# Performance work log

Measured on AMD Instinct MI355X. Metric: run time of the kernel, lower is better.

## Reference

```python
import jax, jax.numpy as jnp
import numpy as np

NG, N, NFG, NFR, NFP, B = 4, 64, 1024, 256, 256, 2048
SCALE = 1.0 / float(np.sqrt(NFR + NFP))
EPS = 1e-5  # torch LayerNorm default


def setup_inputs() -> dict:
    key = jax.random.key(0)
    k = jax.random.split(key, 4)
    x = jax.random.normal(k[0], (B, N, NFG), dtype=jnp.float32)
    # per-graph params stacked over NG for vectorized computation
    Wt = jax.random.normal(k[1], (NG, NFR, NFG), dtype=jnp.float32) * 0.02
    bt = jnp.zeros((NG, NFR), dtype=jnp.float32)
    Wp = jax.random.normal(k[2], (NG, NFR, NFG), dtype=jnp.float32) * 0.02
    bp = jnp.zeros((NG, NFR), dtype=jnp.float32)
    Wg = jax.random.normal(k[3], (NG, NFG, NFG), dtype=jnp.float32) * 0.02  # [out,in]
    gamma = jnp.ones((NG, NFG), dtype=jnp.float32)
    beta = jnp.zeros((NG, NFG), dtype=jnp.float32)
    return {"x": x, "Wt": Wt, "bt": bt, "Wp": Wp, "bp": bp,
            "Wg": Wg, "gamma": gamma, "beta": beta}


def reference(x, Wt, bt, Wp, bp, Wg, gamma, beta):
    # theta/phi projections, vectorized over NG graphs: [G,B,N,R]
    theta = jnp.einsum('bnf,grf->gbnr', x, Wt) + bt[:, None, None, :]
    phi = jnp.einsum('bnf,grf->gbnr', x, Wp) + bp[:, None, None, :]
    # original computes sim=theta@phi^T then .sum(2); identical math:
    # relation[b,n] = theta[b,n] . sum_m phi[b,m]  (avoids the NxN matrix)
    phi_sum = phi.sum(axis=2)                                  # [G,B,R]
    relation = jnp.einsum('gbnr,gbr->gbn', theta, phi_sum) * SCALE
    w = jax.nn.softmax(relation, axis=2)                       # softmax over boxes N
    # attention-weighted aggregation over boxes -> [G,B,NFG]
    agg = jnp.einsum('gbn,bnf->gbf', w, x)
    # GCN linear (no bias): [G,B,NFG]
    h = jnp.einsum('gbf,gof->gbo', agg, Wg)
    # LayerNorm over feature dim, per graph
    mu = h.mean(axis=-1, keepdims=True)
    var = ((h - mu) ** 2).mean(axis=-1, keepdims=True)
    h = (h - mu) * jax.lax.rsqrt(var + EPS) * gamma[:, None, :] + beta[:, None, :]
    h = jax.nn.relu(h)
    # mean over the NG graphs; restore keepdim axis -> [B,1,NFG]
    return h.mean(axis=0)[:, None, :]
```

## Files before the change

kernel.cpp:

```cpp
#include <hip/hip_runtime.h>
#include <hip/hip_bf16.h>

typedef __attribute__((ext_vector_type(4))) float f4;
typedef __attribute__((ext_vector_type(4))) float f32x4;
typedef __attribute__((ext_vector_type(8))) short short8;
typedef __attribute__((ext_vector_type(2))) unsigned int u32x2;
typedef __attribute__((ext_vector_type(4))) unsigned int u32x4;
typedef unsigned int u32;
typedef unsigned short u16;

#define SCALE_F 0.04419417382415922f

__device__ inline u16 f2bf(float f) {
  u32 u = __float_as_uint(f);
  u32 r = u + 0x7FFFu + ((u >> 16) & 1u);
  return (u16)(r >> 16);
}
__device__ inline float bflo(u32 u) { return __uint_as_float(u << 16); }
__device__ inline float bfhi(u32 u) { return __uint_as_float(u & 0xFFFF0000u); }

#define GLD16(gsrc, ldst)                                                     \
  __builtin_amdgcn_global_load_lds(                                           \
      (const __attribute__((address_space(1))) void*)(gsrc),                  \
      (__attribute__((address_space(3))) void*)(ldst), 16, 0, 0)

__global__ __launch_bounds__(256) void k0_cvt(const float* __restrict__ src,
                                              u16* __restrict__ dst) {
  int i = blockIdx.x * 256 + threadIdx.x;
  const f4* s = (const f4*)src;
  f4 a = s[(size_t)i * 2];
  f4 b = s[(size_t)i * 2 + 1];
  u32x4 p;
  p[0] = (u32)f2bf(a[0]) | ((u32)f2bf(a[1]) << 16);
  p[1] = (u32)f2bf(a[2]) | ((u32)f2bf(a[3]) << 16);
  p[2] = (u32)f2bf(b[0]) | ((u32)f2bf(b[1]) << 16);
  p[3] = (u32)f2bf(b[2]) | ((u32)f2bf(b[3]) << 16);
  *(u32x4*)(dst + (size_t)i * 8) = p;
}

__global__ __launch_bounds__(256) void k0_wt(const float* __restrict__ Wt,
                                             u16* __restrict__ Wtt) {
  const int g = blockIdx.z;
  const int f0 = blockIdx.x * 64, r0 = blockIdx.y * 64;
  __shared__ u16 tile[64][66];
  const int t = threadIdx.x;
  const float* src = Wt + ((size_t)g * 256 + r0) * 1024 + f0;
#pragma unroll
  for (int i = 0; i < 16; ++i) {
    int idx = t + i * 256;
    int rl = idx >> 6, fl = idx & 63;
    tile[fl][rl] = f2bf(src[rl * 1024 + fl]);
  }
  __syncthreads();
  u16* dst = Wtt + ((size_t)g * 1024 + f0) * 256 + r0;
#pragma unroll
  for (int i = 0; i < 4; ++i) {
    int idx = t + i * 256;
    int fl = idx >> 4, rq = idx & 15;
    u32x2 p;
    p[0] = (u32)tile[fl][rq * 4]     | ((u32)tile[fl][rq * 4 + 1] << 16);
    p[1] = (u32)tile[fl][rq * 4 + 2] | ((u32)tile[fl][rq * 4 + 3] << 16);
    *(u32x2*)(dst + fl * 256 + rq * 4) = p;
  }
}

__global__ __launch_bounds__(256) void k1_colsum(const float* __restrict__ x,
                                                 u16* __restrict__ xs16) {
  int b = blockIdx.x, t = threadIdx.x;
  const float* xb = x + (size_t)b * (64 * 1024);
  f4 acc = {0.f, 0.f, 0.f, 0.f};
#pragma unroll 8
  for (int n = 0; n < 64; ++n)
    acc += *(const f4*)(xb + n * 1024 + t * 4);
  u32x2 p;
  p[0] = (u32)f2bf(acc[0]) | ((u32)f2bf(acc[1]) << 16);
  p[1] = (u32)f2bf(acc[2]) | ((u32)f2bf(acc[3]) << 16);
  *(u32x2*)(xs16 + (size_t)b * 1024 + t * 4) = p;
}

__global__ __launch_bounds__(256) void k2_gemm(const u16* __restrict__ A,
                                               const u16* __restrict__ Bt,
                                               const float* __restrict__ bp,
                                               u16* __restrict__ C) {
  const int n0 = blockIdx.x * 128, m0 = blockIdx.y * 128;
  __shared__ u16 Al[128 * 32];
  __shared__ u16 Bl[128 * 32];
  const int t = threadIdx.x;
  const int w = t >> 6, l = t & 63;
  const int wr = w >> 1, wc = w & 1;
  const int lr = l & 15, lh = l >> 4;
  f32x4 acc[4][4] = {};
  for (int kt = 0; kt < 1024; kt += 32) {
#pragma unroll
    for (int j = 0; j < 2; ++j) {
      int idx = t + j * 256;
      int row = idx >> 2, sl = idx & 3;
      GLD16(A + (size_t)(m0 + row) * 1024 + kt + sl * 8, Al + idx * 8);
      GLD16(Bt + (size_t)(n0 + row) * 1024 + kt + sl * 8, Bl + idx * 8);
    }
    __syncthreads();
    short8 af[4], bfr[4];
#pragma unroll
    for (int m = 0; m < 4; ++m)
      af[m] = *(const short8*)(Al + (wr * 64 + m * 16 + lr) * 32 + lh * 8);
#pragma unroll
    for (int n = 0; n < 4; ++n)
      bfr[n] = *(const short8*)(Bl + (wc * 64 + n * 16 + lr) * 32 + lh * 8);
#pragma unroll
    for (int m = 0; m < 4; ++m)
#pragma unroll
      for (int n = 0; n < 4; ++n)
        acc[m][n] = __builtin_amdgcn_mfma_f32_16x16x32_bf16(af[m], bfr[n],
                                                            acc[m][n], 0, 0, 0);
    __syncthreads();
  }
#pragma unroll
  for (int m = 0; m < 4; ++m)
#pragma unroll
    for (int n = 0; n < 4; ++n) {
      int col = n0 + wc * 64 + n * 16 + lr;
      float bb = 64.0f * bp[col];
#pragma unroll
      for (int j = 0; j < 4; ++j)
        C[(size_t)(m0 + wr * 64 + m * 16 + lh * 4 + j) * 1024 + col] =
            f2bf(acc[m][n][j] + bb);
    }
}

__global__ __launch_bounds__(256) void k3_gemm(const u16* __restrict__ A,
                                               const u16* __restrict__ Btt,
                                               float* __restrict__ V) {
  const int g = blockIdx.z;
  const int n0 = blockIdx.x * 128, m0 = blockIdx.y * 128;
  const u16* Bg = Btt + (size_t)g * 1024 * 256;
  __shared__ u16 Al[128 * 32];
  __shared__ u16 Bl[128 * 32];
  const int t = threadIdx.x;
  const int w = t >> 6, l = t & 63;
  const int wr = w >> 1, wc = w & 1;
  const int lr = l & 15, lh = l >> 4;
  f32x4 acc[4][4] = {};
  for (int kt = 0; kt < 256; kt += 32) {
#pragma unroll
    for (int j = 0; j < 2; ++j) {
      int idx = t + j * 256;
      int row = idx >> 2, sl = idx & 3;
      GLD16(A + (size_t)(m0 + row) * 1024 + g * 256 + kt + sl * 8, Al + idx * 8);
      GLD16(Bg + (size_t)(n0 + row) * 256 + kt + sl * 8, Bl + idx * 8);
    }
    __syncthreads();
    short8 af[4], bfr[4];
#pragma unroll
    for (int m = 0; m < 4; ++m)
      af[m] = *(const short8*)(Al + (wr * 64 + m * 16 + lr) * 32 + lh * 8);
#pragma unroll
    for (int n = 0; n < 4; ++n)
      bfr[n] = *(const short8*)(Bl + (wc * 64 + n * 16 + lr) * 32 + lh * 8);
#pragma unroll
    for (int m = 0; m < 4; ++m)
#pragma unroll
      for (int n = 0; n < 4; ++n)
        acc[m][n] = __builtin_amdgcn_mfma_f32_16x16x32_bf16(af[m], bfr[n],
                                                            acc[m][n], 0, 0, 0);
    __syncthreads();
  }
  float* Vg = V + (size_t)g * 2048 * 1024;
#pragma unroll
  for (int m = 0; m < 4; ++m)
#pragma unroll
    for (int n = 0; n < 4; ++n)
#pragma unroll
      for (int j = 0; j < 4; ++j)
        Vg[(size_t)(m0 + wr * 64 + m * 16 + lh * 4 + j) * 1024 +
           (n0 + wc * 64 + n * 16 + lr)] = acc[m][n][j];
}

#define K4_LDS (131072 + 16384 + 8192 + 1024)
__global__ __launch_bounds__(1024) void k4_fused(const float* __restrict__ x,
                                                 const float* __restrict__ V,
                                                 u16* __restrict__ aggb) {
  extern __shared__ char sm[];
  char* xl = sm;
  float* vl = (float*)(sm + 131072);
  float* relp = (float*)(sm + 131072 + 16384);
  float* wsm = (float*)(sm + 131072 + 16384 + 8192);
  const int t = threadIdx.x;
  const int b = blockIdx.x;
  const float* xb = x + (size_t)b * 65536;

  f4 va = *(const f4*)(V + ((size_t)(t >> 8) * 2048 + b) * 1024 + (t & 255) * 4);
  f4 xr[8];
#pragma unroll
  for (int i = 0; i < 8; ++i) {
    int idx = i * 1024 + t;
    xr[i] = *(const f4*)(xb + (idx >> 8) * 1024 + (idx & 255) * 4);
  }
  *(f4*)(vl + t * 4) = va;
#pragma unroll
  for (int i = 0; i < 8; ++i) {
    int idx = i * 1024 + t;
    int row = idx >> 8, col4 = idx & 255;
    u32 p0 = (u32)f2bf(xr[i][0]) | ((u32)f2bf(xr[i][1]) << 16);
    u32 p1 = (u32)f2bf(xr[i][2]) | ((u32)f2bf(xr[i][3]) << 16);
    int slot = col4 >> 1, half = col4 & 1;
    char* dst = xl + row * 2048 + ((slot ^ (row & 7)) << 4) + half * 8;
    ((u32*)dst)[0] = p0;
    ((u32*)dst)[1] = p1;
  }
  f4 xr2[8];
#pragma unroll
  for (int i = 0; i < 8; ++i) {
    int idx = 8192 + i * 1024 + t;
    xr2[i] = *(const f4*)(xb + (idx >> 8) * 1024 + (idx & 255) * 4);
  }
  asm volatile("s_waitcnt lgkmcnt(0)" ::: "memory");
  __builtin_amdgcn_s_barrier();

  {
    const int h = t >> 7, g = (t >> 5) & 3, n = t & 31;
    const char* xrow = xl + n * 2048;
    const float* vg = vl + g * 1024 + h * 128;
    const int sw = n & 7;
    float racc = 0.f;
#pragma unroll
    for (int f8 = 0; f8 < 16; ++f8) {
      int slot = h * 16 + f8;
      u32x4 xp = *(const u32x4*)(xrow + ((slot ^ sw) << 4));
      f4 v0 = *(const f4*)(vg + f8 * 8);
      f4 v1 = *(const f4*)(vg + f8 * 8 + 4);
      racc = fmaf(bflo(xp[0]), v0[0], racc);
      racc = fmaf(bfhi(xp[0]), v0[1], racc);
      racc = fmaf(bflo(xp[1]), v0[2], racc);
      racc = fmaf(bfhi(xp[1]), v0[3], racc);
      racc = fmaf(bflo(xp[2]), v1[0], racc);
      racc = fmaf(bfhi(xp[2]), v1[1], racc);
      racc = fmaf(bflo(xp[3]), v1[2], racc);
      racc = fmaf(bfhi(xp[3]), v1[3], racc);
    }
    relp[t] = racc;
  }
#pragma unroll
  for (int i = 0; i < 8; ++i) {
    int idx = 8192 + i * 1024 + t;
    int row = idx >> 8, col4 = idx & 255;
    u32 p0 = (u32)f2bf(xr2[i][0]) | ((u32)f2bf(xr2[i][1]) << 16);
    u32 p1 = (u32)f2bf(xr2[i][2]) | ((u32)f2bf(xr2[i][3]) << 16);
    int slot = col4 >> 1, half = col4 & 1;
    char* dst = xl + row * 2048 + ((slot ^ (row & 7)) << 4) + half * 8;
    ((u32*)dst)[0] = p0;
    ((u32*)dst)[1] = p1;
  }
  asm volatile("s_waitcnt lgkmcnt(0)" ::: "memory");
  __builtin_amdgcn_s_barrier();

  {
    const int h = t >> 7, g = (t >> 5) & 3, n = 32 + (t & 31);
    const char* xrow = xl + n * 2048;
    const float* vg = vl + g * 1024 + h * 128;
    const int sw = n & 7;
    float racc = 0.f;
#pragma unroll
    for (int f8 = 0; f8 < 16; ++f8) {
      int slot = h * 16 + f8;
      u32x4 xp = *(const u32x4*)(xrow + ((slot ^ sw) << 4));
      f4 v0 = *(const f4*)(vg + f8 * 8);
      f4 v1 = *(const f4*)(vg + f8 * 8 + 4);
      racc = fmaf(bflo(xp[0]), v0[0], racc);
      racc = fmaf(bfhi(xp[0]), v0[1], racc);
      racc = fmaf(bflo(xp[1]), v0[2], racc);
      racc = fmaf(bfhi(xp[1]), v0[3], racc);
      racc = fmaf(bflo(xp[2]), v1[0], racc);
      racc = fmaf(bfhi(xp[2]), v1[1], racc);
      racc = fmaf(bflo(xp[3]), v1[2], racc);
      racc = fmaf(bfhi(xp[3]), v1[3], racc);
    }
    relp[1024 + t] = racc;
  }
  __syncthreads();

  if (t < 256) {
    const int g = t >> 6, n = t & 63;
    const float* base = (n < 32) ? (relp + g * 32 + (n & 31))
                                 : (relp + 1024 + g * 32 + (n & 31));
    float rel = 0.f;
#pragma unroll
    for (int h = 0; h < 8; ++h) rel += base[h * 128];
    rel *= SCALE_F;
    float mx = rel;
#pragma unroll
    for (int o = 32; o > 0; o >>= 1) mx = fmaxf(mx, __shfl_xor(mx, o, 64));
    float e = __expf(rel - mx);
    float s = e;
#pragma unroll
    for (int o = 32; o > 0; o >>= 1) s += __shfl_xor(s, o, 64);
    wsm[t] = e / s;
  }
  __syncthreads();

  {
    const int g = t >> 8, fb4 = t & 255;
    const float* wg = wsm + g * 64;
    const int slot = fb4 >> 1, half = fb4 & 1;
    float a0 = 0, a1 = 0, a2 = 0, a3 = 0;
#pragma unroll 8
    for (int n = 0; n < 64; ++n) {
      float w = wg[n];
      u32x2 xp = *(const u32x2*)(xl + n * 2048 + ((slot ^ (n & 7)) << 4) + half * 8);
      a0 = fmaf(bflo(xp[0]), w, a0);
      a1 = fmaf(bfhi(xp[0]), w, a1);
      a2 = fmaf(bflo(xp[1]), w, a2);
      a3 = fmaf(bfhi(xp[1]), w, a3);
    }
    u32x2 p;
    p[0] = (u32)f2bf(a0) | ((u32)f2bf(a1) << 16);
    p[1] = (u32)f2bf(a2) | ((u32)f2bf(a3) << 16);
    *(u32x2*)(aggb + ((size_t)g * 2048 + b) * 1024 + fb4 * 4) = p;
  }
}

__global__ __launch_bounds__(256) void k5_gemm(const u16* __restrict__ Ab,
                                               const u16* __restrict__ Bb,
                                               float* __restrict__ H) {
  const int g = blockIdx.z;
  const int n0 = blockIdx.x * 128, m0 = blockIdx.y * 128;
  const u16* A = Ab + (size_t)g * 2048 * 1024;
  const u16* Bt = Bb + (size_t)g * 1024 * 1024;
  __shared__ u16 Al[128 * 32];
  __shared__ u16 Bl[128 * 32];
  const int t = threadIdx.x;
  const int w = t >> 6, l = t & 63;
  const int wr = w >> 1, wc = w & 1;
  const int lr = l & 15, lh = l >> 4;
  f32x4 acc[4][4] = {};
  for (int kt = 0; kt < 1024; kt += 32) {
#pragma unroll
    for (int j = 0; j < 2; ++j) {
      int idx = t + j * 256;
      int row = idx >> 2, sl = idx & 3;
      GLD16(A + (size_t)(m0 + row) * 1024 + kt + sl * 8, Al + idx * 8);
      GLD16(Bt + (size_t)(n0 + row) * 1024 + kt + sl * 8, Bl + idx * 8);
    }
    __syncthreads();
    short8 af[4], bfr[4];
#pragma unroll
    for (int m = 0; m < 4; ++m)
      af[m] = *(const short8*)(Al + (wr * 64 + m * 16 + lr) * 32 + lh * 8);
#pragma unroll
    for (int n = 0; n < 4; ++n)
      bfr[n] = *(const short8*)(Bl + (wc * 64 + n * 16 + lr) * 32 + lh * 8);
#pragma unroll
    for (int m = 0; m < 4; ++m)
#pragma unroll
      for (int n = 0; n < 4; ++n)
        acc[m][n] = __builtin_amdgcn_mfma_f32_16x16x32_bf16(af[m], bfr[n],
                                                            acc[m][n], 0, 0, 0);
    __syncthreads();
  }
  float* Hg = H + (size_t)g * 2048 * 1024;
#pragma unroll
  for (int m = 0; m < 4; ++m)
#pragma unroll
    for (int n = 0; n < 4; ++n)
#pragma unroll
      for (int j = 0; j < 4; ++j)
        Hg[(size_t)(m0 + wr * 64 + m * 16 + lh * 4 + j) * 1024 +
           (n0 + wc * 64 + n * 16 + lr)] = acc[m][n][j];
}

__global__ __launch_bounds__(256) void k6_ln(const float* __restrict__ H,
                                             const float* __restrict__ gamma,
                                             const float* __restrict__ beta,
                                             float* __restrict__ out) {
  const int b = blockIdx.x, t = threadIdx.x;
  const int w = t >> 6, lane = t & 63;
  __shared__ float red[8];
  f4 acc = {0.f, 0.f, 0.f, 0.f};
  for (int g = 0; g < 4; ++g) {
    f4 hv = *(const f4*)(H + ((size_t)g * 2048 + b) * 1024 + t * 4);
    float s = hv[0] + hv[1] + hv[2] + hv[3];
    float q = hv[0] * hv[0] + hv[1] * hv[1] + hv[2] * hv[2] + hv[3] * hv[3];
#pragma unroll
    for (int o = 32; o > 0; o >>= 1) {
      s += __shfl_xor(s, o, 64);
      q += __shfl_xor(q, o, 64);
    }
    if (lane == 0) { red[w] = s; red[4 + w] = q; }
    __syncthreads();
    s = red[0] + red[1] + red[2] + red[3];
    q = red[4] + red[5] + red[6] + red[7];
    float mean = s * (1.f / 1024.f);
    float var = q * (1.f / 1024.f) - mean * mean;
    float rstd = rsqrtf(var + 1e-5f);
    f4 gm = *(const f4*)(gamma + g * 1024 + t * 4);
    f4 bt = *(const f4*)(beta + g * 1024 + t * 4);
#pragma unroll
    for (int j = 0; j < 4; ++j) {
      float val = (hv[j] - mean) * rstd * gm[j] + bt[j];
      acc[j] += fmaxf(val, 0.f);
    }
    __syncthreads();
  }
  acc *= 0.25f;
  *(f4*)(out + (size_t)b * 1024 + t * 4) = acc;
}

extern "C" void kernel_launch(void* const* d_in, const int* in_sizes, int n_in,
                              void* d_out, int out_size, void* d_ws, size_t ws_size,
                              hipStream_t stream) {
  const float* x     = (const float*)d_in[0];
  const float* Wt    = (const float*)d_in[1];
  const float* Wp    = (const float*)d_in[3];
  const float* bp    = (const float*)d_in[4];
  const float* Wg    = (const float*)d_in[5];
  const float* gamma = (const float*)d_in[6];
  const float* beta  = (const float*)d_in[7];
  float* out = (float*)d_out;

  char* ws = (char*)d_ws;
  u16*   xs16 = (u16*)(ws);
  u16*   ps16 = (u16*)(ws + (4u << 20));
  u16*   wpb  = (u16*)(ws + (8u << 20));
  u16*   wtb  = (u16*)(ws + (10u << 20));
  u16*   wgb  = (u16*)(ws + (12u << 20));
  float* v    = (float*)(ws + (20u << 20));
  float* h    = (float*)(ws + (20u << 20));
  u16*   aggb = (u16*)(ws + (52u << 20));

  hipFuncSetAttribute((const void*)k4_fused,
                      hipFuncAttributeMaxDynamicSharedMemorySize, K4_LDS);

  k0_cvt<<<2048, 256, 0, stream>>>(Wg, wgb);
  k0_cvt<<<512, 256, 0, stream>>>(Wp, wpb);
  k0_wt<<<dim3(16, 4, 4), 256, 0, stream>>>(Wt, wtb);
  k1_colsum<<<2048, 256, 0, stream>>>(x, xs16);
  k2_gemm<<<dim3(8, 16), 256, 0, stream>>>(xs16, wpb, bp, ps16);
  k3_gemm<<<dim3(8, 16, 4), 256, 0, stream>>>(ps16, wtb, v);
  k4_fused<<<2048, 1024, K4_LDS, stream>>>(x, v, aggb);
  k5_gemm<<<dim3(8, 16, 4), 256, 0, stream>>>(aggb, wgb, h);
  k6_ln<<<2048, 256, 0, stream>>>(h, gamma, beta, out);
}
```

Measured before the change: 358.8 us.

## Compute k4 relation scores with MFMA and split aggregation over box halves

```diff
diff --git a/kernel.cpp b/kernel.cpp
--- a/kernel.cpp
+++ b/kernel.cpp
@@ -175,31 +175,30 @@
            (n0 + wc * 64 + n * 16 + lr)] = acc[m][n][j];
 }
 
-#define K4_LDS (131072 + 16384 + 8192 + 1024)
+#define K4_LDS (131072 + 8256 + 16384 + 1024)
 __global__ __launch_bounds__(1024) void k4_fused(const float* __restrict__ x,
                                                  const float* __restrict__ V,
                                                  u16* __restrict__ aggb) {
   extern __shared__ char sm[];
   char* xl = sm;
-  float* vl = (float*)(sm + 131072);
-  float* relp = (float*)(sm + 131072 + 16384);
-  float* wsm = (float*)(sm + 131072 + 16384 + 8192);
+  u16* vb = (u16*)(sm + 131072);
+  float* relp = (float*)(sm + 139328);
+  float* wsm = (float*)(sm + 155712);
   const int t = threadIdx.x;
   const int b = blockIdx.x;
   const float* xb = x + (size_t)b * 65536;
 
+  f4 xr[8];
+#pragma unroll
+  for (int i = 0; i < 8; ++i) {
+    int u = i * 1024 + t;
+    xr[i] = *(const f4*)(xb + (u >> 7) * 1024 + (u & 127) * 4);
+  }
   f4 va = *(const f4*)(V + ((size_t)(t >> 8) * 2048 + b) * 1024 + (t & 255) * 4);
-  f4 xr[8];
 #pragma unroll
   for (int i = 0; i < 8; ++i) {
-    int idx = i * 1024 + t;
-    xr[i] = *(const f4*)(xb + (idx >> 8) * 1024 + (idx & 255) * 4);
-  }
-  *(f4*)(vl + t * 4) = va;
-#pragma unroll
-  for (int i = 0; i < 8; ++i) {
-    int idx = i * 1024 + t;
-    int row = idx >> 8, col4 = idx & 255;
+    int u = i * 1024 + t;
+    int row = u >> 7, col4 = u & 127;
     u32 p0 = (u32)f2bf(xr[i][0]) | ((u32)f2bf(xr[i][1]) << 16);
     u32 p1 = (u32)f2bf(xr[i][2]) | ((u32)f2bf(xr[i][3]) << 16);
     int slot = col4 >> 1, half = col4 & 1;
@@ -207,42 +206,42 @@
     ((u32*)dst)[0] = p0;
     ((u32*)dst)[1] = p1;
   }
+  {
+    int g = t >> 8, q = t & 255;
+    u32x2 p;
+    p[0] = (u32)f2bf(va[0]) | ((u32)f2bf(va[1]) << 16);
+    p[1] = (u32)f2bf(va[2]) | ((u32)f2bf(va[3]) << 16);
+    *(u32x2*)(vb + g * 1032 + q * 4) = p;
+  }
   f4 xr2[8];
 #pragma unroll
   for (int i = 0; i < 8; ++i) {
-    int idx = 8192 + i * 1024 + t;
-    xr2[i] = *(const f4*)(xb + (idx >> 8) * 1024 + (idx & 255) * 4);
+    int u = i * 1024 + t;
+    xr2[i] = *(const f4*)(xb + (u >> 7) * 1024 + (u & 127) * 4 + 512);
   }
   asm volatile("s_waitcnt lgkmcnt(0)" ::: "memory");
   __builtin_amdgcn_s_barrier();
 
+  const int w = t >> 6, l = t & 63, lg = l >> 4, lr = l & 15;
+  f32x4 racc[4] = {};
   {
-    const int h = t >> 7, g = (t >> 5) & 3, n = t & 31;
-    const char* xrow = xl + n * 2048;
-    const float* vg = vl + g * 1024 + h * 128;
-    const int sw = n & 7;
-    float racc = 0.f;
-#pragma unroll
-    for (int f8 = 0; f8 < 16; ++f8) {
-      int slot = h * 16 + f8;
-      u32x4 xp = *(const u32x4*)(xrow + ((slot ^ sw) << 4));
-      f4 v0 = *(const f4*)(vg + f8 * 8);
-      f4 v1 = *(const f4*)(vg + f8 * 8 + 4);
-      racc = fmaf(bflo(xp[0]), v0[0], racc);
-      racc = fmaf(bfhi(xp[0]), v0[1], racc);
-      racc = fmaf(bflo(xp[1]), v0[2], racc);
-      racc = fmaf(bfhi(xp[1]), v0[3], racc);
-      racc = fmaf(bflo(xp[2]), v1[0], racc);
-      racc = fmaf(bfhi(xp[2]), v1[1], racc);
-      racc = fmaf(bflo(xp[3]), v1[2], racc);
-      racc = fmaf(bfhi(xp[3]), v1[3], racc);
-    }
-    relp[t] = racc;
+    const int kt = w * 32;
+    short8 afr = {};
+    if (lr < 4)
+      afr = *(const short8*)(vb + lr * 1032 + kt + lg * 8);
+#pragma unroll
+    for (int nt = 0; nt < 4; ++nt) {
+      int n = nt * 16 + lr;
+      short8 bfrg = *(const short8*)(
+          xl + n * 2048 + ((((kt >> 3) + lg) ^ (n & 7)) << 4));
+      racc[nt] = __builtin_amdgcn_mfma_f32_16x16x32_bf16(afr, bfrg, racc[nt],
+                                                         0, 0, 0);
+    }
   }
 #pragma unroll
   for (int i = 0; i < 8; ++i) {
-    int idx = 8192 + i * 1024 + t;
-    int row = idx >> 8, col4 = idx & 255;
+    int u = i * 1024 + t;
+    int row = u >> 7, col4 = 128 + (u & 127);
     u32 p0 = (u32)f2bf(xr2[i][0]) | ((u32)f2bf(xr2[i][1]) << 16);
     u32 p1 = (u32)f2bf(xr2[i][2]) | ((u32)f2bf(xr2[i][3]) << 16);
     int slot = col4 >> 1, half = col4 & 1;
@@ -254,37 +253,33 @@
   __builtin_amdgcn_s_barrier();
 
   {
-    const int h = t >> 7, g = (t >> 5) & 3, n = 32 + (t & 31);
-    const char* xrow = xl + n * 2048;
-    const float* vg = vl + g * 1024 + h * 128;
-    const int sw = n & 7;
-    float racc = 0.f;
-#pragma unroll
-    for (int f8 = 0; f8 < 16; ++f8) {
-      int slot = h * 16 + f8;
-      u32x4 xp = *(const u32x4*)(xrow + ((slot ^ sw) << 4));
-      f4 v0 = *(const f4*)(vg + f8 * 8);
-      f4 v1 = *(const f4*)(vg + f8 * 8 + 4);
-      racc = fmaf(bflo(xp[0]), v0[0], racc);
-      racc = fmaf(bfhi(xp[0]), v0[1], racc);
-      racc = fmaf(bflo(xp[1]), v0[2], racc);
-      racc = fmaf(bfhi(xp[1]), v0[3], racc);
-      racc = fmaf(bflo(xp[2]), v1[0], racc);
-      racc = fmaf(bfhi(xp[2]), v1[1], racc);
-      racc = fmaf(bflo(xp[3]), v1[2], racc);
-      racc = fmaf(bfhi(xp[3]), v1[3], racc);
-    }
-    relp[1024 + t] = racc;
+    const int kt = 512 + w * 32;
+    short8 afr = {};
+    if (lr < 4)
+      afr = *(const short8*)(vb + lr * 1032 + kt + lg * 8);
+#pragma unroll
+    for (int nt = 0; nt < 4; ++nt) {
+      int n = nt * 16 + lr;
+      short8 bfrg = *(const short8*)(
+          xl + n * 2048 + ((((kt >> 3) + lg) ^ (n & 7)) << 4));
+      racc[nt] = __builtin_amdgcn_mfma_f32_16x16x32_bf16(afr, bfrg, racc[nt],
+                                                         0, 0, 0);
+    }
+  }
+  if (l < 16) {
+#pragma unroll
+    for (int nt = 0; nt < 4; ++nt)
+#pragma unroll
+      for (int j = 0; j < 4; ++j)
+        relp[(w * 4 + j) * 64 + nt * 16 + lr] = racc[nt][j];
   }
   __syncthreads();
 
   if (t < 256) {
     const int g = t >> 6, n = t & 63;
-    const float* base = (n < 32) ? (relp + g * 32 + (n & 31))
-                                 : (relp + 1024 + g * 32 + (n & 31));
     float rel = 0.f;
 #pragma unroll
-    for (int h = 0; h < 8; ++h) rel += base[h * 128];
+    for (int ww = 0; ww < 16; ++ww) rel += relp[(ww * 4 + g) * 64 + n];
     rel *= SCALE_F;
     float mx = rel;
 #pragma unroll
@@ -298,23 +293,40 @@
   __syncthreads();
 
   {
-    const int g = t >> 8, fb4 = t & 255;
-    const float* wg = wsm + g * 64;
-    const int slot = fb4 >> 1, half = fb4 & 1;
-    float a0 = 0, a1 = 0, a2 = 0, a3 = 0;
+    const int hh = t >> 9, r = t & 511, g = r >> 7, f8 = r & 127;
+    const float* wg = wsm + g * 64 + hh * 32;
+    float a0 = 0, a1 = 0, a2 = 0, a3 = 0, a4 = 0, a5 = 0, a6 = 0, a7 = 0;
 #pragma unroll 8
-    for (int n = 0; n < 64; ++n) {
-      float w = wg[n];
-      u32x2 xp = *(const u32x2*)(xl + n * 2048 + ((slot ^ (n & 7)) << 4) + half * 8);
-      a0 = fmaf(bflo(xp[0]), w, a0);
-      a1 = fmaf(bfhi(xp[0]), w, a1);
-      a2 = fmaf(bflo(xp[1]), w, a2);
-      a3 = fmaf(bfhi(xp[1]), w, a3);
-    }
-    u32x2 p;
-    p[0] = (u32)f2bf(a0) | ((u32)f2bf(a1) << 16);
-    p[1] = (u32)f2bf(a2) | ((u32)f2bf(a3) << 16);
-    *(u32x2*)(aggb + ((size_t)g * 2048 + b) * 1024 + fb4 * 4) = p;
+    for (int n0 = 0; n0 < 32; ++n0) {
+      int n = hh * 32 + n0;
+      float wv = wg[n0];
+      u32x4 xp = *(const u32x4*)(xl + n * 2048 + ((f8 ^ (n & 7)) << 4));
+      a0 = fmaf(bflo(xp[0]), wv, a0);
+      a1 = fmaf(bfhi(xp[0]), wv, a1);
+      a2 = fmaf(bflo(xp[1]), wv, a2);
+      a3 = fmaf(bfhi(xp[1]), wv, a3);
+      a4 = fmaf(bflo(xp[2]), wv, a4);
+      a5 = fmaf(bfhi(xp[2]), wv, a5);
+      a6 = fmaf(bflo(xp[3]), wv, a6);
+      a7 = fmaf(bfhi(xp[3]), wv, a7);
+    }
+    if (hh) {
+      f4 q0 = {a0, a1, a2, a3};
+      f4 q1 = {a4, a5, a6, a7};
+      *(f4*)(relp + r * 8) = q0;
+      *(f4*)(relp + r * 8 + 4) = q1;
+    }
+    __syncthreads();
+    if (!hh) {
+      f4 q0 = *(const f4*)(relp + r * 8);
+      f4 q1 = *(const f4*)(relp + r * 8 + 4);
+      u32x4 p;
+      p[0] = (u32)f2bf(a0 + q0[0]) | ((u32)f2bf(a1 + q0[1]) << 16);
+      p[1] = (u32)f2bf(a2 + q0[2]) | ((u32)f2bf(a3 + q0[3]) << 16);
+      p[2] = (u32)f2bf(a4 + q1[0]) | ((u32)f2bf(a5 + q1[1]) << 16);
+      p[3] = (u32)f2bf(a6 + q1[2]) | ((u32)f2bf(a7 + q1[3]) << 16);
+      *(u32x4*)(aggb + ((size_t)g * 2048 + b) * 1024 + f8 * 8) = p;
+    }
   }
 }
 
```

After: 349.7 us. 2.5% less time.
